# Optimization experiments

Measured on AMD Instinct MI355X. Metric: run time of the kernel, lower is better.

Reference implementation:

```python
import jax, jax.numpy as jnp
import numpy as np

N, T, H, E = 16384, 4, 64, 262144
NEG_SLOPE = 0.2  # LeakyReLU slope for GAT-style attention
LN_EPS = 1e-5


def setup_inputs() -> dict:
    key = jax.random.key(0)
    ks = jax.random.split(key, 24)
    p = {}
    p["pred"] = jax.random.normal(ks[0], (N, T, H), jnp.float32)
    p["ei_structural"] = jax.random.randint(ks[1], (2, E), 0, N, jnp.int32)
    p["ei_functional"] = jax.random.randint(ks[2], (2, E), 0, N, jnp.int32)
    scale = 1.0 / np.sqrt(H)
    i = 3
    for l in range(2):
        for et in ("s", "f"):
            p[f"W{l}{et}"] = (jax.random.normal(ks[i], (H, H), jnp.float32) * scale); i += 1
            p[f"a{l}{et}"] = (jax.random.normal(ks[i], (H,), jnp.float32) * scale); i += 1
        p[f"g{l}"] = jnp.ones((H,), jnp.float32)
        p[f"b{l}"] = jnp.zeros((H,), jnp.float32)
    return p


def _conv(x, ei, W, a, n_dst):
    """Attention-based ST graph conv, temporal_kernel_size=1 (per-step)."""
    h = jnp.einsum('nth,hd->ntd', x, W)          # [N,T,H] linear transform
    src, dst = ei[0], ei[1]
    he = h[src]                                   # [E,T,H] gather per edge
    logits = jax.nn.leaky_relu(jnp.einsum('eth,h->et', he, a), NEG_SLOPE)
    m = jax.ops.segment_max(logits, dst, num_segments=n_dst)     # [N,T]
    ex = jnp.exp(logits - m[dst])                 # stable softmax over incoming edges
    den = jax.ops.segment_sum(ex, dst, num_segments=n_dst)
    alpha = ex / den[dst]                         # [E,T]
    return jax.ops.segment_sum(alpha[..., None] * he, dst, num_segments=n_dst)


def _ln(x, g, b):
    mu = x.mean(-1, keepdims=True)
    v = x.var(-1, keepdims=True)
    return (x - mu) * jax.lax.rsqrt(v + LN_EPS) * g + b


def reference(pred, ei_structural, ei_functional,
              W0s, a0s, W0f, a0f, g0, b0,
              W1s, a1s, W1f, a1f, g1, b1):
    x = pred
    layers = ((W0s, a0s, W0f, a0f, g0, b0), (W1s, a1s, W1f, a1f, g1, b1))
    for (Ws, av, Wf, af, g, b) in layers:
        ms = _conv(x, ei_structural, Ws, av, N)
        mf = _conv(x, ei_functional, Wf, af, N)
        # sum(messages)/len(messages), residual, LayerNorm over H (dropout=identity in eval)
        x = _ln(x + 0.5 * (ms + mf), g, b)
    return x
```

## Files before the change

### kernel.cpp

```cpp
#include <hip/hip_runtime.h>
#include <hip/hip_bf16.h>

#define NN 16384
#define TT 4
#define HH 64
#define NT (NN * TT)
#define NEG_SLOPE 0.2f
#define LN_EPS 1e-5f

typedef __attribute__((ext_vector_type(8))) short short8;
typedef __attribute__((ext_vector_type(4))) float f32x4;

__device__ __forceinline__ float bf2f(unsigned short u) {
    return __uint_as_float((unsigned)u << 16);
}
__device__ __forceinline__ unsigned short f2bf(float f) {
    unsigned u = __float_as_uint(f);
    return (unsigned short)((u + 0x7FFF + ((u >> 16) & 1)) >> 16);
}


__global__ void zero_kernel(int* __restrict__ a, int n) {
    int i = blockIdx.x * blockDim.x + threadIdx.x;
    if (i < n) a[i] = 0;
}

__global__ void hist2_kernel(const int* __restrict__ dst_s, const int* __restrict__ dst_f,
                             int* __restrict__ cnt2, int E) {
    int e = blockIdx.x * blockDim.x + threadIdx.x;
    if (e < E) {
        atomicAdd(&cnt2[dst_s[e]], 1);
    } else {
        e -= E;
        if (e < E) atomicAdd(&cnt2[NN + dst_f[e]], 1);
    }
}

__global__ __launch_bounds__(1024) void scan2_kernel(const int* __restrict__ cnt2,
                                                     int* __restrict__ rp2,
                                                     int* __restrict__ cur2) {
    __shared__ int part[1024];
    const int set = blockIdx.x;
    const int* cnt = cnt2 + set * NN;
    int* rp = rp2 + set * (NN + 1);
    int* cur = cur2 + set * NN;
    int tid = threadIdx.x;
    int base = tid * 16;
    int local[16];
    int sum = 0;
#pragma unroll
    for (int i = 0; i < 16; i++) { local[i] = cnt[base + i]; sum += local[i]; }
    part[tid] = sum;
    __syncthreads();
    for (int off = 1; off < 1024; off <<= 1) {
        int v = (tid >= off) ? part[tid - off] : 0;
        __syncthreads();
        part[tid] += v;
        __syncthreads();
    }
    int run = (tid == 0) ? 0 : part[tid - 1];
#pragma unroll
    for (int i = 0; i < 16; i++) {
        rp[base + i] = run;
        cur[base + i] = run;
        run += local[i];
    }
    if (tid == 1023) rp[NN] = run;
}

__global__ void scatter2_kernel(const int* __restrict__ ei_s, const int* __restrict__ ei_f,
                                int* __restrict__ cur2, int* __restrict__ col2, int E) {
    int e = blockIdx.x * blockDim.x + threadIdx.x;
    if (e < E) {
        int d = ei_s[E + e];
        int pos = atomicAdd(&cur2[d], 1);
        col2[pos] = ei_s[e];
    } else {
        e -= E;
        if (e < E) {
            int d = ei_f[E + e];
            int pos = atomicAdd(&cur2[NN + d], 1);
            col2[E + pos] = ei_f[e];
        }
    }
}


__global__ __launch_bounds__(256) void transform2_kernel(
    const float4* __restrict__ x4,
    const float* __restrict__ Ws, const float* __restrict__ as_,
    const float* __restrict__ Wf, const float* __restrict__ af,
    unsigned short* __restrict__ h_s, float* __restrict__ sc_s,
    unsigned short* __restrict__ h_f, float* __restrict__ sc_f) {
    const int lane = threadIdx.x & 63;
    const int wv = threadIdx.x >> 6;
    const int m = lane & 15;
    const int quad = lane >> 4;

    short8 Bs[4][2], Bf[4][2];
#pragma unroll
    for (int c = 0; c < 4; c++) {
#pragma unroll
        for (int ks = 0; ks < 2; ks++) {
#pragma unroll
            for (int j = 0; j < 8; j++) {
                int k = ks * 32 + quad * 8 + j;
                int n = c * 16 + m;
                Bs[c][ks][j] = (short)f2bf(Ws[k * 64 + n]);
                Bf[c][ks][j] = (short)f2bf(Wf[k * 64 + n]);
            }
        }
    }
    float a_s[4], a_f[4];
#pragma unroll
    for (int c = 0; c < 4; c++) { a_s[c] = as_[c * 16 + m]; a_f[c] = af[c * 16 + m]; }

    const int rowbase = blockIdx.x * 128 + wv * 32;
#pragma unroll
    for (int rt = 0; rt < 2; rt++) {
        const int row0 = rowbase + rt * 16;
        const long xbase = (long)(row0 + m) * 16 + quad * 2;
        float4 xa = x4[xbase];
        float4 xb = x4[xbase + 1];
        float4 xc = x4[xbase + 8];
        float4 xd = x4[xbase + 9];
        short8 A0, A1;
        A0[0] = (short)f2bf(xa.x); A0[1] = (short)f2bf(xa.y);
        A0[2] = (short)f2bf(xa.z); A0[3] = (short)f2bf(xa.w);
        A0[4] = (short)f2bf(xb.x); A0[5] = (short)f2bf(xb.y);
        A0[6] = (short)f2bf(xb.z); A0[7] = (short)f2bf(xb.w);
        A1[0] = (short)f2bf(xc.x); A1[1] = (short)f2bf(xc.y);
        A1[2] = (short)f2bf(xc.z); A1[3] = (short)f2bf(xc.w);
        A1[4] = (short)f2bf(xd.x); A1[5] = (short)f2bf(xd.y);
        A1[6] = (short)f2bf(xd.z); A1[7] = (short)f2bf(xd.w);

        f32x4 accs[4], accf[4];
#pragma unroll
        for (int c = 0; c < 4; c++) {
            accs[c] = (f32x4){0.f, 0.f, 0.f, 0.f};
            accf[c] = (f32x4){0.f, 0.f, 0.f, 0.f};
        }
#pragma unroll
        for (int c = 0; c < 4; c++) {
            accs[c] = __builtin_amdgcn_mfma_f32_16x16x32_bf16(A0, Bs[c][0], accs[c], 0, 0, 0);
            accs[c] = __builtin_amdgcn_mfma_f32_16x16x32_bf16(A1, Bs[c][1], accs[c], 0, 0, 0);
            accf[c] = __builtin_amdgcn_mfma_f32_16x16x32_bf16(A0, Bf[c][0], accf[c], 0, 0, 0);
            accf[c] = __builtin_amdgcn_mfma_f32_16x16x32_bf16(A1, Bf[c][1], accf[c], 0, 0, 0);
        }
#pragma unroll
        for (int reg = 0; reg < 4; reg++) {
            const int row = row0 + quad * 4 + reg;
            float ps = 0.f, pf = 0.f;
#pragma unroll
            for (int c = 0; c < 4; c++) {
                h_s[(long)row * 64 + c * 16 + m] = f2bf(accs[c][reg]);
                h_f[(long)row * 64 + c * 16 + m] = f2bf(accf[c][reg]);
                ps = fmaf(accs[c][reg], a_s[c], ps);
                pf = fmaf(accf[c][reg], a_f[c], pf);
            }
#pragma unroll
            for (int off = 1; off < 16; off <<= 1) {
                ps += __shfl_xor(ps, off, 64);
                pf += __shfl_xor(pf, off, 64);
            }
            if (m == 0) {
                sc_s[row] = (ps > 0.f) ? ps : NEG_SLOPE * ps;
                sc_f[row] = (pf > 0.f) ? pf : NEG_SLOPE * pf;
            }
        }
    }
}


__device__ __forceinline__ void agg_set(const ushort4* __restrict__ h4,
                                        const float* __restrict__ sc,
                                        const int* __restrict__ rp,
                                        const int* __restrict__ col,
                                        int n, int t, int lane, float4& msg) {
    const int beg = rp[n], end = rp[n + 1];
    float den = 0.f;
    float ax = 0.f, ay = 0.f, az = 0.f, aw = 0.f;
    int j = beg;
    for (; j + 8 <= end; j += 8) {
        int s[8];
        float l[8];
        ushort4 hh[8];
#pragma unroll
        for (int u = 0; u < 8; u++) s[u] = col[j + u];
#pragma unroll
        for (int u = 0; u < 8; u++) l[u] = sc[s[u] * 4 + t];
#pragma unroll
        for (int u = 0; u < 8; u++) hh[u] = h4[s[u] * 64 + lane];
#pragma unroll
        for (int u = 0; u < 8; u++) {
            float e = __expf(l[u]);
            den += e;
            ax = fmaf(e, bf2f(hh[u].x), ax);
            ay = fmaf(e, bf2f(hh[u].y), ay);
            az = fmaf(e, bf2f(hh[u].z), az);
            aw = fmaf(e, bf2f(hh[u].w), aw);
        }
    }
    for (; j + 4 <= end; j += 4) {
        int s[4];
        float l[4];
        ushort4 hh[4];
#pragma unroll
        for (int u = 0; u < 4; u++) s[u] = col[j + u];
#pragma unroll
        for (int u = 0; u < 4; u++) l[u] = sc[s[u] * 4 + t];
#pragma unroll
        for (int u = 0; u < 4; u++) hh[u] = h4[s[u] * 64 + lane];
#pragma unroll
        for (int u = 0; u < 4; u++) {
            float e = __expf(l[u]);
            den += e;
            ax = fmaf(e, bf2f(hh[u].x), ax);
            ay = fmaf(e, bf2f(hh[u].y), ay);
            az = fmaf(e, bf2f(hh[u].z), az);
            aw = fmaf(e, bf2f(hh[u].w), aw);
        }
    }
    for (; j < end; j++) {
        int s0 = col[j];
        float l0 = sc[s0 * 4 + t];
        ushort4 h0 = h4[s0 * 64 + lane];
        float e0 = __expf(l0);
        den += e0;
        ax = fmaf(e0, bf2f(h0.x), ax);
        ay = fmaf(e0, bf2f(h0.y), ay);
        az = fmaf(e0, bf2f(h0.z), az);
        aw = fmaf(e0, bf2f(h0.w), aw);
    }
    if (end > beg) {
        float r = 1.f / den;
        msg.x = ax * r; msg.y = ay * r; msg.z = az * r; msg.w = aw * r;
    } else {
        msg.x = msg.y = msg.z = msg.w = 0.f;
    }
}

__global__ __launch_bounds__(256) void aggregate_kernel(
    const float4* __restrict__ x4,
    const ushort4* __restrict__ hs4, const float* __restrict__ scs,
    const int* __restrict__ rps, const int* __restrict__ cols,
    const ushort4* __restrict__ hf4, const float* __restrict__ scf,
    const int* __restrict__ rpf, const int* __restrict__ colf,
    const float4* __restrict__ g4, const float4* __restrict__ b4,
    float4* __restrict__ out4) {
    const int wv = threadIdx.x >> 6;
    const int lane = threadIdx.x & 63;
    const int n = blockIdx.x * 4 + wv;
    const int t = lane >> 4;
    const int ci = lane & 15;

    float4 xv = x4[n * 64 + lane];

    float4 ms, mf;
    agg_set(hs4, scs, rps, cols, n, t, lane, ms);
    agg_set(hf4, scf, rpf, colf, n, t, lane, mf);

    float v0 = xv.x + 0.5f * (ms.x + mf.x);
    float v1 = xv.y + 0.5f * (ms.y + mf.y);
    float v2 = xv.z + 0.5f * (ms.z + mf.z);
    float v3 = xv.w + 0.5f * (ms.w + mf.w);

    float sum = (v0 + v1) + (v2 + v3);
#pragma unroll
    for (int off = 1; off < 16; off <<= 1) sum += __shfl_xor(sum, off, 64);
    float mu = sum * (1.f / 64.f);
    float d0 = v0 - mu, d1 = v1 - mu, d2 = v2 - mu, d3 = v3 - mu;
    float var = (d0 * d0 + d1 * d1) + (d2 * d2 + d3 * d3);
#pragma unroll
    for (int off = 1; off < 16; off <<= 1) var += __shfl_xor(var, off, 64);
    var *= (1.f / 64.f);
    float inv = rsqrtf(var + LN_EPS);
    float4 gv = g4[ci], bv = b4[ci];
    float4 o;
    o.x = d0 * inv * gv.x + bv.x;
    o.y = d1 * inv * gv.y + bv.y;
    o.z = d2 * inv * gv.z + bv.z;
    o.w = d3 * inv * gv.w + bv.w;
    out4[n * 64 + lane] = o;
}


extern "C" void kernel_launch(void* const* d_in, const int* in_sizes, int n_in,
                              void* d_out, int out_size, void* d_ws, size_t ws_size,
                              hipStream_t stream) {
    const float* pred = (const float*)d_in[0];
    const int* ei_s = (const int*)d_in[1];
    const int* ei_f = (const int*)d_in[2];
    const float* W0s = (const float*)d_in[3];
    const float* a0s = (const float*)d_in[4];
    const float* W0f = (const float*)d_in[5];
    const float* a0f = (const float*)d_in[6];
    const float* g0  = (const float*)d_in[7];
    const float* b0  = (const float*)d_in[8];
    const float* W1s = (const float*)d_in[9];
    const float* a1s = (const float*)d_in[10];
    const float* W1f = (const float*)d_in[11];
    const float* a1f = (const float*)d_in[12];
    const float* g1  = (const float*)d_in[13];
    const float* b1  = (const float*)d_in[14];
    const int E = in_sizes[1] / 2;

    char* ws = (char*)d_ws;
    auto alloc = [&](size_t bytes) {
        char* p = ws;
        ws += (bytes + 255) & ~(size_t)255;
        return p;
    };
    int* cnt2 = (int*)alloc((size_t)2 * NN * sizeof(int));
    int* rp2  = (int*)alloc((size_t)2 * (NN + 1) * sizeof(int));
    int* cur2 = (int*)alloc((size_t)2 * NN * sizeof(int));
    int* col2 = (int*)alloc((size_t)2 * E * sizeof(int));
    unsigned short* h_s = (unsigned short*)alloc((size_t)NT * HH * sizeof(unsigned short));
    unsigned short* h_f = (unsigned short*)alloc((size_t)NT * HH * sizeof(unsigned short));
    float* sc_s = (float*)alloc((size_t)NT * sizeof(float));
    float* sc_f = (float*)alloc((size_t)NT * sizeof(float));
    float* x_mid = (float*)alloc((size_t)NT * HH * sizeof(float));

    const int* rp_s = rp2;
    const int* rp_f = rp2 + (NN + 1);
    const int* col_s = col2;
    const int* col_f = col2 + E;

    const int EB = (E + 255) / 256;

    zero_kernel<<<(2 * NN) / 256, 256, 0, stream>>>(cnt2, 2 * NN);
    hist2_kernel<<<2 * EB, 256, 0, stream>>>(ei_s + E, ei_f + E, cnt2, E);
    scan2_kernel<<<2, 1024, 0, stream>>>(cnt2, rp2, cur2);
    scatter2_kernel<<<2 * EB, 256, 0, stream>>>(ei_s, ei_f, cur2, col2, E);

    transform2_kernel<<<NT / 128, 256, 0, stream>>>(
        (const float4*)pred, W0s, a0s, W0f, a0f, h_s, sc_s, h_f, sc_f);
    aggregate_kernel<<<NN / 4, 256, 0, stream>>>(
        (const float4*)pred, (const ushort4*)h_s, sc_s, rp_s, col_s,
        (const ushort4*)h_f, sc_f, rp_f, col_f,
        (const float4*)g0, (const float4*)b0, (float4*)x_mid);

    transform2_kernel<<<NT / 128, 256, 0, stream>>>(
        (const float4*)x_mid, W1s, a1s, W1f, a1f, h_s, sc_s, h_f, sc_f);
    aggregate_kernel<<<NN / 4, 256, 0, stream>>>(
        (const float4*)x_mid, (const ushort4*)h_s, sc_s, rp_s, col_s,
        (const ushort4*)h_f, sc_f, rp_f, col_f,
        (const float4*)g1, (const float4*)b1, (float4*)d_out);
}
```

Measured before the change: 256.0 us.

## Parallelize CSR offset scan and split aggregation sets across waves

The old two-block, 1024-thread scan with its serial shared-memory loop is replaced by three kernels. A per-block reduce is followed by a single-block wave-level scan of the 128 partials, where each 64-lane wave handles one edge set. A final pass uses wave shuffles to produce row pointers and cursors. The aggregate kernel now gives the structural and functional edge sets to separate waves of each node and combines them through shared memory, so the two gather loops run in parallel rather than back to back. This adds two extra launches, a block barrier, and half-idle waves during the LayerNorm tail.

```diff
diff --git a/kernel.cpp b/kernel.cpp
--- a/kernel.cpp
+++ b/kernel.cpp
@@ -36,36 +36,60 @@
     }
 }
 
-__global__ __launch_bounds__(1024) void scan2_kernel(const int* __restrict__ cnt2,
-                                                     int* __restrict__ rp2,
-                                                     int* __restrict__ cur2) {
-    __shared__ int part[1024];
-    const int set = blockIdx.x;
-    const int* cnt = cnt2 + set * NN;
+__global__ __launch_bounds__(256) void scanA_kernel(const int* __restrict__ cnt2,
+                                                    int* __restrict__ partial) {
+    __shared__ int wsum[4];
+    const int lane = threadIdx.x & 63;
+    const int wv = threadIdx.x >> 6;
+    int v = cnt2[blockIdx.x * 256 + threadIdx.x];
+#pragma unroll
+    for (int off = 32; off > 0; off >>= 1) v += __shfl_xor(v, off, 64);
+    if (lane == 0) wsum[wv] = v;
+    __syncthreads();
+    if (threadIdx.x == 0)
+        partial[blockIdx.x] = wsum[0] + wsum[1] + wsum[2] + wsum[3];
+}
+
+__global__ __launch_bounds__(128) void scanB_kernel(int* __restrict__ partial) {
+    const int lane = threadIdx.x & 63;
+    int v = partial[threadIdx.x];
+    int inc = v;
+#pragma unroll
+    for (int off = 1; off < 64; off <<= 1) {
+        int t = __shfl_up(inc, off, 64);
+        if (lane >= off) inc += t;
+    }
+    partial[threadIdx.x] = inc - v;
+}
+
+__global__ __launch_bounds__(256) void scanC_kernel(const int* __restrict__ cnt2,
+                                                    const int* __restrict__ partial,
+                                                    int* __restrict__ rp2,
+                                                    int* __restrict__ cur2) {
+    __shared__ int wsum[4];
+    const int lane = threadIdx.x & 63;
+    const int wv = threadIdx.x >> 6;
+    const int gidx = blockIdx.x * 256 + threadIdx.x;
+    const int set = gidx >> 14;
+    const int i = gidx & (NN - 1);
+    int v = cnt2[gidx];
+    int inc = v;
+#pragma unroll
+    for (int off = 1; off < 64; off <<= 1) {
+        int t = __shfl_up(inc, off, 64);
+        if (lane >= off) inc += t;
+    }
+    if (lane == 63) wsum[wv] = inc;
+    __syncthreads();
+    int wbase = 0;
+#pragma unroll
+    for (int w = 0; w < 4; w++)
+        if (w < wv) wbase += wsum[w];
+    int excl = (inc - v) + wbase + partial[blockIdx.x];
     int* rp = rp2 + set * (NN + 1);
-    int* cur = cur2 + set * NN;
-    int tid = threadIdx.x;
-    int base = tid * 16;
-    int local[16];
-    int sum = 0;
-#pragma unroll
-    for (int i = 0; i < 16; i++) { local[i] = cnt[base + i]; sum += local[i]; }
-    part[tid] = sum;
-    __syncthreads();
-    for (int off = 1; off < 1024; off <<= 1) {
-        int v = (tid >= off) ? part[tid - off] : 0;
-        __syncthreads();
-        part[tid] += v;
-        __syncthreads();
-    }
-    int run = (tid == 0) ? 0 : part[tid - 1];
-#pragma unroll
-    for (int i = 0; i < 16; i++) {
-        rp[base + i] = run;
-        cur[base + i] = run;
-        run += local[i];
-    }
-    if (tid == 1023) rp[NN] = run;
+    rp[i] = excl;
+    cur2[gidx] = excl;
+    if (i == NN - 1) rp[NN] = excl + v;
 }
 
 __global__ void scatter2_kernel(const int* __restrict__ ei_s, const int* __restrict__ ei_f,
@@ -248,22 +272,32 @@
     const int* __restrict__ rpf, const int* __restrict__ colf,
     const float4* __restrict__ g4, const float4* __restrict__ b4,
     float4* __restrict__ out4) {
+    __shared__ float4 msgF[2][64];
     const int wv = threadIdx.x >> 6;
     const int lane = threadIdx.x & 63;
-    const int n = blockIdx.x * 4 + wv;
+    const int slot = wv >> 1;
+    const int set = wv & 1;
+    const int n = blockIdx.x * 2 + slot;
     const int t = lane >> 4;
     const int ci = lane & 15;
 
+    float4 msg;
+    if (set == 0) {
+        agg_set(hs4, scs, rps, cols, n, t, lane, msg);
+    } else {
+        agg_set(hf4, scf, rpf, colf, n, t, lane, msg);
+        msgF[slot][lane] = msg;
+    }
+    __syncthreads();
+    if (set == 1) return;
+
+    float4 mf = msgF[slot][lane];
     float4 xv = x4[n * 64 + lane];
 
-    float4 ms, mf;
-    agg_set(hs4, scs, rps, cols, n, t, lane, ms);
-    agg_set(hf4, scf, rpf, colf, n, t, lane, mf);
-
-    float v0 = xv.x + 0.5f * (ms.x + mf.x);
-    float v1 = xv.y + 0.5f * (ms.y + mf.y);
-    float v2 = xv.z + 0.5f * (ms.z + mf.z);
-    float v3 = xv.w + 0.5f * (ms.w + mf.w);
+    float v0 = xv.x + 0.5f * (msg.x + mf.x);
+    float v1 = xv.y + 0.5f * (msg.y + mf.y);
+    float v2 = xv.z + 0.5f * (msg.z + mf.z);
+    float v3 = xv.w + 0.5f * (msg.w + mf.w);
 
     float sum = (v0 + v1) + (v2 + v3);
 #pragma unroll
@@ -315,6 +349,7 @@
     int* rp2  = (int*)alloc((size_t)2 * (NN + 1) * sizeof(int));
     int* cur2 = (int*)alloc((size_t)2 * NN * sizeof(int));
     int* col2 = (int*)alloc((size_t)2 * E * sizeof(int));
+    int* partial = (int*)alloc(128 * sizeof(int));
     unsigned short* h_s = (unsigned short*)alloc((size_t)NT * HH * sizeof(unsigned short));
     unsigned short* h_f = (unsigned short*)alloc((size_t)NT * HH * sizeof(unsigned short));
     float* sc_s = (float*)alloc((size_t)NT * sizeof(float));
@@ -330,19 +365,21 @@
 
     zero_kernel<<<(2 * NN) / 256, 256, 0, stream>>>(cnt2, 2 * NN);
     hist2_kernel<<<2 * EB, 256, 0, stream>>>(ei_s + E, ei_f + E, cnt2, E);
-    scan2_kernel<<<2, 1024, 0, stream>>>(cnt2, rp2, cur2);
+    scanA_kernel<<<128, 256, 0, stream>>>(cnt2, partial);
+    scanB_kernel<<<1, 128, 0, stream>>>(partial);
+    scanC_kernel<<<128, 256, 0, stream>>>(cnt2, partial, rp2, cur2);
     scatter2_kernel<<<2 * EB, 256, 0, stream>>>(ei_s, ei_f, cur2, col2, E);
 
     transform2_kernel<<<NT / 128, 256, 0, stream>>>(
         (const float4*)pred, W0s, a0s, W0f, a0f, h_s, sc_s, h_f, sc_f);
-    aggregate_kernel<<<NN / 4, 256, 0, stream>>>(
+    aggregate_kernel<<<NN / 2, 256, 0, stream>>>(
         (const float4*)pred, (const ushort4*)h_s, sc_s, rp_s, col_s,
         (const ushort4*)h_f, sc_f, rp_f, col_f,
         (const float4*)g0, (const float4*)b0, (float4*)x_mid);
 
     transform2_kernel<<<NT / 128, 256, 0, stream>>>(
         (const float4*)x_mid, W1s, a1s, W1f, a1f, h_s, sc_s, h_f, sc_f);
-    aggregate_kernel<<<NN / 4, 256, 0, stream>>>(
+    aggregate_kernel<<<NN / 2, 256, 0, stream>>>(
         (const float4*)x_mid, (const ushort4*)h_s, sc_s, rp_s, col_s,
         (const ushort4*)h_f, sc_f, rp_f, col_f,
         (const float4*)g1, (const float4*)b1, (float4*)d_out);
```

Measured after the change: 254.0 us. Within noise of the previous version (-0.8%).
